# Optimization experiments

Measured on AMD Instinct MI355X. Metric: run time of the kernel, lower is better.

The kernel has to match this reference:

```python
import jax, jax.numpy as jnp
import numpy as np

N_NODES = 50000
N_EDGES = 800000
NUM_RELATIONS = 8   # 2 * n_speakers**2 with n_speakers = 2
NUM_BASES = 30
G_DIM, H1_DIM, H2_DIM = 128, 128, 128


def setup_inputs() -> dict:
    key = jax.random.key(0)
    ks = jax.random.split(key, 10)
    inp = {
        "node_features": jax.random.normal(ks[0], (N_NODES, G_DIM), jnp.float32),
        "edge_index": jax.random.randint(ks[1], (2, N_EDGES), 0, N_NODES, dtype=jnp.int64),
        "edge_type": jax.random.randint(ks[2], (N_EDGES,), 0, NUM_RELATIONS, dtype=jnp.int64),
        "edge_norm": jax.random.uniform(ks[3], (N_EDGES,), jnp.float32),
        # RGCNConv params (basis decomposition)
        "basis": jax.random.normal(ks[4], (NUM_BASES, G_DIM, H1_DIM), jnp.float32) * 0.05,
        "comp": jax.random.normal(ks[5], (NUM_RELATIONS, NUM_BASES), jnp.float32) * 0.1,
        "root": jax.random.normal(ks[6], (G_DIM, H1_DIM), jnp.float32) * 0.05,
        "bias1": jnp.zeros((H1_DIM,), jnp.float32),
        # GraphConv params: lin_rel (with bias) applied to aggregated neighbors, lin_root (no bias)
        "w_rel": jax.random.normal(ks[7], (H1_DIM, H2_DIM), jnp.float32) * 0.05,
        "b_rel": jnp.zeros((H2_DIM,), jnp.float32),
        "w_root": jax.random.normal(ks[8], (H1_DIM, H2_DIM), jnp.float32) * 0.05,
    }
    return inp


def reference(node_features, edge_index, edge_type, edge_norm,
              basis, comp, root, bias1, w_rel, b_rel, w_root):
    src, dst = edge_index[0], edge_index[1]  # source_to_target flow (PyG default)

    # ---- Layer 1: RGCNConv with basis decomposition ----
    # W[r] = sum_b comp[r,b] * basis[b]  -> [R, g, h1]
    W = jnp.einsum('rb,bio->rio', comp, basis)
    # Project every node under every relation once (N*R*h1), then gather per edge.
    # Mathematically identical to per-edge x_j @ W[edge_type] but avoids an [E, g, h1] tensor.
    x_proj = jnp.einsum('ni,rio->nro', node_features, W)  # [N, R, h1]
    msg = x_proj[src, edge_type] * edge_norm[:, None]     # [E, h1]
    agg = jax.ops.segment_sum(msg, dst, num_segments=N_NODES)  # scatter-add to targets
    h = agg + node_features @ root + bias1                # [N, h1]

    # ---- Layer 2: GraphConv (aggr='add', no edge_weight) ----
    agg2 = jax.ops.segment_sum(h[src], dst, num_segments=N_NODES)  # [N, h1]
    out = agg2 @ w_rel + b_rel + h @ w_root               # [N, h2]
    return out
```

## Files before the change

### kernel.cpp

```cpp
#include <hip/hip_runtime.h>
#include <hip/hip_bf16.h>
#include <stdint.h>

#define N_NODES 50000
#define N_EDGES 800000
#define NREL    8
#define NBASES  30
#define DIM     128
#define NSLOT   9
#define NCAT    (NSLOT*DIM)
#define SCAN_NB ((N_NODES + 255) / 256)
#define NB_C    196
#define EPB_PLACE 2048
#define NBLK_PLACE ((N_EDGES + EPB_PLACE - 1) / EPB_PLACE)

typedef __attribute__((ext_vector_type(8))) short short8;
typedef __attribute__((ext_vector_type(4))) float floatx4;
typedef __hip_bfloat16  bf16;
typedef __hip_bfloat162 bf16x2;

__device__ inline ushort f2bu(float f) { bf16 b = __float2bfloat16(f); return *(ushort*)&b; }
__device__ inline float  bu2f(ushort u) { union { unsigned i; float f; } c; c.i = ((unsigned)u) << 16; return c.f; }

__global__ void prep_weights(const float* __restrict__ basis, const float* __restrict__ comp,
                             const float* __restrict__ root, const float* __restrict__ w_rel,
                             const float* __restrict__ w_root,
                             bf16* __restrict__ WcatT, bf16* __restrict__ wrelT, bf16* __restrict__ wrootT) {
    int idx = blockIdx.x * blockDim.x + threadIdx.x;
    const int n_cat = NCAT * DIM;
    const int n_sq  = DIM * DIM;
    if (idx < n_cat) {
        int k = idx & 127, n = idx >> 7;
        int r = n >> 7, o = n & 127;
        float v;
        if (r < NREL) {
            v = 0.f;
            for (int b = 0; b < NBASES; ++b)
                v += comp[r * NBASES + b] * basis[(b * DIM + k) * DIM + o];
        } else {
            v = root[k * DIM + o];
        }
        WcatT[n * DIM + k] = __float2bfloat16(v);
    } else if (idx < n_cat + n_sq) {
        int t = idx - n_cat; int k = t & 127, o = t >> 7;
        wrelT[o * DIM + k] = __float2bfloat16(w_rel[k * DIM + o]);
    } else if (idx < n_cat + 2 * n_sq) {
        int t = idx - n_cat - n_sq; int k = t & 127, o = t >> 7;
        wrootT[o * DIM + k] = __float2bfloat16(w_root[k * DIM + o]);
    }
}

__global__ void conv_x(const float4* __restrict__ x4, ushort4* __restrict__ xb4, int n4) {
    int i = blockIdx.x * blockDim.x + threadIdx.x;
    if (i < n4) {
        float4 f = x4[i];
        ushort4 o;
        o.x = f2bu(f.x); o.y = f2bu(f.y); o.z = f2bu(f.z); o.w = f2bu(f.w);
        xb4[i] = o;
    }
}

__global__ void hist_kernel(const int* __restrict__ ei, int* __restrict__ deg) {
    int e = blockIdx.x * blockDim.x + threadIdx.x;
    if (e < N_EDGES) atomicAdd(&deg[ei[N_EDGES + e]], 1);
}

__global__ void scan_blocks(const int* __restrict__ deg, int* __restrict__ segoff,
                            int* __restrict__ bsum, int n) {
    __shared__ int buf[256];
    int tid = threadIdx.x;
    int i = blockIdx.x * 256 + tid;
    int v = (i < n) ? deg[i] : 0;
    buf[tid] = v;
    __syncthreads();
#pragma unroll
    for (int o = 1; o < 256; o <<= 1) {
        int t = (tid >= o) ? buf[tid - o] : 0;
        __syncthreads();
        buf[tid] += t;
        __syncthreads();
    }
    if (i < n) segoff[i + 1] = buf[tid];
    if (tid == 255) bsum[blockIdx.x] = buf[255];
}

__global__ void scan_sums(int* __restrict__ bsum, int nb) {
    int lane = threadIdx.x;
    int base = 0;
    for (int start = 0; start < nb; start += 64) {
        int i = start + lane;
        int v = (i < nb) ? bsum[i] : 0;
        int incl = v;
#pragma unroll
        for (int o = 1; o < 64; o <<= 1) {
            int t = __shfl_up(incl, o, 64);
            if (lane >= o) incl += t;
        }
        if (i < nb) bsum[i] = base + incl - v;
        base += __shfl(incl, 63, 64);
    }
}

__global__ void scan_add(int* __restrict__ segoff, const int* __restrict__ bsum, int n) {
    int i = blockIdx.x * 256 + threadIdx.x;
    if (i < n) segoff[i + 1] += bsum[blockIdx.x];
    if (i == 0) segoff[0] = 0;
}

__global__ __launch_bounds__(256) void place_kernel(const int* __restrict__ ei, const int* __restrict__ et,
                                                    const float* __restrict__ en, const int* __restrict__ segoff,
                                                    int* __restrict__ bcur, uint2* __restrict__ tmp) {
    __shared__ int lhist[NB_C];
    __shared__ int lbase[NB_C];
    __shared__ int lrank[NB_C];
    int tid = threadIdx.x;
    for (int i = tid; i < NB_C; i += 256) { lhist[i] = 0; lrank[i] = 0; }
    __syncthreads();
    int e0 = blockIdx.x * EPB_PLACE;
#pragma unroll
    for (int i = 0; i < EPB_PLACE / 256; ++i) {
        int e = e0 + i * 256 + tid;
        if (e < N_EDGES) atomicAdd(&lhist[ei[N_EDGES + e] >> 8], 1);
    }
    __syncthreads();
    for (int c = tid; c < NB_C; c += 256)
        if (lhist[c] > 0) lbase[c] = atomicAdd(&bcur[c], lhist[c]);
    __syncthreads();
#pragma unroll
    for (int i = 0; i < EPB_PLACE / 256; ++i) {
        int e = e0 + i * 256 + tid;
        if (e < N_EDGES) {
            int d = ei[N_EDGES + e];
            int c = d >> 8;
            int r = atomicAdd(&lrank[c], 1);
            int p = segoff[c << 8] + lbase[c] + r;
            tmp[p] = make_uint2((unsigned)ei[e] | ((unsigned)et[e] << 16) | ((unsigned)(d & 255) << 19),
                                __float_as_uint(en[e]));
        }
    }
}

__global__ __launch_bounds__(256) void sortb_kernel(const uint2* __restrict__ tmp, const int* __restrict__ segoff,
                                                    uint2* __restrict__ rec) {
    __shared__ int cur[256];
    int c = blockIdx.x;
    int tid = threadIdx.x;
    cur[tid] = 0;
    __syncthreads();
    int base = segoff[c << 8];
    int nlimit = (c + 1) << 8; if (nlimit > N_NODES) nlimit = N_NODES;
    int end = segoff[nlimit];
    for (int i = base + tid; i < end; i += 256) {
        uint2 r = tmp[i];
        int dl = (r.x >> 19) & 255;
        int p = segoff[(c << 8) + dl] + atomicAdd(&cur[dl], 1);
        rec[p] = make_uint2(r.x & 0x7FFFFu, r.y);
    }
}

__global__ __launch_bounds__(256) void gemm1_kernel(const bf16* __restrict__ A, const bf16* __restrict__ BT,
                                                    bf16* __restrict__ C, int M) {
    __shared__ ushort As[64][136];
    __shared__ ushort Bs[64][136];
    const ushort* Au = (const ushort*)A;
    const ushort* Bu = (const ushort*)BT;
    ushort* Cu = (ushort*)C;
    int tm = blockIdx.x * 64;
    int wave = threadIdx.x >> 6, lane = threadIdx.x & 63;
    int q = lane >> 4, mr = lane & 15;

#pragma unroll
    for (int u = 0; u < 4; ++u) {
        int cc = threadIdx.x + u * 256;
        int row = cc >> 4, seg = cc & 15;
        int gr = tm + row;
        short8 av = {0, 0, 0, 0, 0, 0, 0, 0};
        if (gr < M) av = *(const short8*)(Au + (size_t)gr * 128 + seg * 8);
        *(short8*)(&As[row][seg * 8]) = av;
    }

    floatx4 zero = {0.f, 0.f, 0.f, 0.f};
    for (int t = 0; t < 18; ++t) {
        if (t) __syncthreads();
#pragma unroll
        for (int u = 0; u < 4; ++u) {
            int cc = threadIdx.x + u * 256;
            int row = cc >> 4, seg = cc & 15;
            short8 bv = *(const short8*)(Bu + (size_t)(t * 64 + row) * 128 + seg * 8);
            *(short8*)(&Bs[row][seg * 8]) = bv;
        }
        __syncthreads();
        floatx4 acc[4] = {zero, zero, zero, zero};
#pragma unroll
        for (int kt = 0; kt < 4; ++kt) {
            short8 a = *(const short8*)(&As[wave * 16 + mr][q * 8 + kt * 32]);
#pragma unroll
            for (int nt = 0; nt < 4; ++nt) {
                short8 b = *(const short8*)(&Bs[nt * 16 + mr][q * 8 + kt * 32]);
                acc[nt] = __builtin_amdgcn_mfma_f32_16x16x32_bf16(a, b, acc[nt], 0, 0, 0);
            }
        }
#pragma unroll
        for (int nt = 0; nt < 4; ++nt)
#pragma unroll
            for (int r4 = 0; r4 < 4; ++r4) {
                int row = tm + wave * 16 + q * 4 + r4;
                if (row < M) Cu[(size_t)row * NCAT + t * 64 + nt * 16 + mr] = f2bu(acc[nt][r4]);
            }
    }
}

__global__ void seg1_kernel(const uint2* __restrict__ rec, const int* __restrict__ segoff,
                            const ushort* __restrict__ proj, const float* __restrict__ bias1,
                            ushort* __restrict__ h) {
    int quad = threadIdx.x >> 4;
    int node = blockIdx.x * 16 + quad;
    if (node >= N_NODES) return;
    int lane = threadIdx.x & 15;
    int s = segoff[node], e = segoff[node + 1];
    float acc[8] = {0.f, 0.f, 0.f, 0.f, 0.f, 0.f, 0.f, 0.f};
    for (int chunk = s; chunk < e; chunk += 4) {
        int m = e - chunk; if (m > 4) m = 4;
        uint2 rr[4]; short8 vv[4];
#pragma unroll
        for (int j = 0; j < 4; ++j) if (j < m) rr[j] = rec[chunk + j];
#pragma unroll
        for (int j = 0; j < 4; ++j) if (j < m) {
            unsigned src = rr[j].x & 0xFFFFu;
            unsigned typ = rr[j].x >> 16;
            vv[j] = *(const short8*)(proj + ((size_t)src * NSLOT + typ) * 128 + lane * 8);
        }
#pragma unroll
        for (int j = 0; j < 4; ++j) if (j < m) {
            float norm = __uint_as_float(rr[j].y);
#pragma unroll
            for (int f = 0; f < 8; ++f) acc[f] += norm * bu2f((ushort)vv[j][f]);
        }
    }
    short8 base = *(const short8*)(proj + ((size_t)node * NSLOT + 8) * 128 + lane * 8);
    short8 o;
#pragma unroll
    for (int f = 0; f < 8; ++f)
        o[f] = (short)f2bu(acc[f] + bu2f((ushort)base[f]) + bias1[lane * 8 + f]);
    *(short8*)(h + (size_t)node * 128 + lane * 8) = o;
}

__global__ void seg2_kernel(const uint2* __restrict__ rec, const int* __restrict__ segoff,
                            const ushort* __restrict__ h, ushort* __restrict__ out2) {
    int quad = threadIdx.x >> 4;
    int node = blockIdx.x * 16 + quad;
    if (node >= N_NODES) return;
    int lane = threadIdx.x & 15;
    int s = segoff[node], e = segoff[node + 1];
    float acc[8] = {0.f, 0.f, 0.f, 0.f, 0.f, 0.f, 0.f, 0.f};
    for (int chunk = s; chunk < e; chunk += 4) {
        int m = e - chunk; if (m > 4) m = 4;
        uint2 rr[4]; short8 vv[4];
#pragma unroll
        for (int j = 0; j < 4; ++j) if (j < m) rr[j] = rec[chunk + j];
#pragma unroll
        for (int j = 0; j < 4; ++j) if (j < m)
            vv[j] = *(const short8*)(h + (size_t)(rr[j].x & 0xFFFFu) * 128 + lane * 8);
#pragma unroll
        for (int j = 0; j < 4; ++j) if (j < m)
#pragma unroll
            for (int f = 0; f < 8; ++f) acc[f] += bu2f((ushort)vv[j][f]);
    }
    short8 o;
#pragma unroll
    for (int f = 0; f < 8; ++f) o[f] = (short)f2bu(acc[f]);
    *(short8*)(out2 + (size_t)node * 128 + lane * 8) = o;
}

__global__ __launch_bounds__(256) void gemm2_kernel(const bf16* __restrict__ A1, const bf16* __restrict__ B1T,
                                                    const bf16* __restrict__ A2, const bf16* __restrict__ B2T,
                                                    const float* __restrict__ brel, float* __restrict__ out, int M) {
    __shared__ ushort As[64][136];
    __shared__ ushort Bs[64][136];
    int tm = blockIdx.x * 64, tn = blockIdx.y * 64;
    int wave = threadIdx.x >> 6, lane = threadIdx.x & 63;
    int q = lane >> 4, mr = lane & 15;
    floatx4 zero = {0.f, 0.f, 0.f, 0.f};
    floatx4 acc[4] = {zero, zero, zero, zero};

    for (int phase = 0; phase < 2; ++phase) {
        const ushort* Au = (const ushort*)(phase ? A2 : A1);
        const ushort* Bu = (const ushort*)(phase ? B2T : B1T);
        if (phase) __syncthreads();
        for (int c = threadIdx.x; c < 64 * 16; c += 256) {
            int row = c >> 4, seg = c & 15;
            int gr = tm + row;
            short8 av = {0, 0, 0, 0, 0, 0, 0, 0};
            if (gr < M) av = *(const short8*)(Au + (size_t)gr * 128 + seg * 8);
            *(short8*)(&As[row][seg * 8]) = av;
            short8 bv = *(const short8*)(Bu + (size_t)(tn + row) * 128 + seg * 8);
            *(short8*)(&Bs[row][seg * 8]) = bv;
        }
        __syncthreads();
#pragma unroll
        for (int kt = 0; kt < 4; ++kt) {
            short8 a = *(const short8*)(&As[wave * 16 + mr][q * 8 + kt * 32]);
#pragma unroll
            for (int nt = 0; nt < 4; ++nt) {
                short8 b = *(const short8*)(&Bs[nt * 16 + mr][q * 8 + kt * 32]);
                acc[nt] = __builtin_amdgcn_mfma_f32_16x16x32_bf16(a, b, acc[nt], 0, 0, 0);
            }
        }
    }
    __syncthreads();
    float* Csf = (float*)&As[0][0];
#pragma unroll
    for (int nt = 0; nt < 4; ++nt)
#pragma unroll
        for (int r4 = 0; r4 < 4; ++r4) {
            int row = wave * 16 + q * 4 + r4;
            int col = nt * 16 + mr;
            Csf[row * 68 + col] = acc[nt][r4] + brel[tn + col];
        }
    __syncthreads();
#pragma unroll
    for (int u = 0; u < 4; ++u) {
        int cc = threadIdx.x + u * 256;
        int row = cc >> 4, seg = cc & 15;
        int gr = tm + row;
        if (gr < M) {
            float4 v = *(const float4*)(&Csf[row * 68 + seg * 4]);
            *(float4*)(out + (size_t)gr * 128 + tn + seg * 4) = v;
        }
    }
}

extern "C" void kernel_launch(void* const* d_in, const int* in_sizes, int n_in,
                              void* d_out, int out_size, void* d_ws, size_t ws_size,
                              hipStream_t stream) {
    const float* x      = (const float*)d_in[0];
    const int*   ei     = (const int*)d_in[1];
    const int*   et     = (const int*)d_in[2];
    const float* en     = (const float*)d_in[3];
    const float* basis  = (const float*)d_in[4];
    const float* comp   = (const float*)d_in[5];
    const float* root   = (const float*)d_in[6];
    const float* bias1  = (const float*)d_in[7];
    const float* w_rel  = (const float*)d_in[8];
    const float* b_rel  = (const float*)d_in[9];
    const float* w_root = (const float*)d_in[10];
    float* out = (float*)d_out;

    char* ws = (char*)d_ws;
    size_t off = 0;
    auto alloc = [&](size_t bytes) { size_t o = off; off += (bytes + 255) & ~(size_t)255; return o; };

    size_t o_deg    = alloc((size_t)N_NODES * 4);
    size_t o_bcur   = alloc((size_t)NB_C * 4);
    size_t o_segoff = alloc((size_t)(N_NODES + 1) * 4);
    size_t o_bsum   = alloc((size_t)SCAN_NB * 4);
    size_t o_rec    = alloc((size_t)N_EDGES * 8);
    size_t o_tmp    = alloc((size_t)N_EDGES * 8);
    size_t o_wcat   = alloc((size_t)NCAT * DIM * 2);
    size_t o_wrel   = alloc((size_t)DIM * DIM * 2);
    size_t o_wroot  = alloc((size_t)DIM * DIM * 2);
    size_t o_xb     = alloc((size_t)N_NODES * DIM * 2);
    size_t o_proj   = alloc((size_t)N_NODES * NCAT * 2);
    size_t o_hb     = alloc((size_t)N_NODES * DIM * 2);
    size_t o_agg2   = alloc((size_t)N_NODES * DIM * 2);

    int*   deg    = (int*)(ws + o_deg);
    int*   bcur   = (int*)(ws + o_bcur);
    int*   segoff = (int*)(ws + o_segoff);
    int*   bsum   = (int*)(ws + o_bsum);
    uint2* rec    = (uint2*)(ws + o_rec);
    uint2* tmp    = (uint2*)(ws + o_tmp);
    bf16*  wcat   = (bf16*)(ws + o_wcat);
    bf16*  wrelT  = (bf16*)(ws + o_wrel);
    bf16*  wrootT = (bf16*)(ws + o_wroot);
    bf16*  xb     = (bf16*)(ws + o_xb);
    bf16*  proj   = (bf16*)(ws + o_proj);
    bf16*  hb     = (bf16*)(ws + o_hb);
    bf16*  agg2   = (bf16*)(ws + o_agg2);

    hipMemsetAsync(ws + o_deg, 0, o_segoff - o_deg, stream);

    {
        int total = NCAT * DIM + 2 * DIM * DIM;
        prep_weights<<<(total + 255) / 256, 256, 0, stream>>>(basis, comp, root, w_rel, w_root,
                                                              wcat, wrelT, wrootT);
    }
    {
        int n4 = N_NODES * DIM / 4;
        conv_x<<<(n4 + 255) / 256, 256, 0, stream>>>((const float4*)x, (ushort4*)xb, n4);
    }
    hist_kernel<<<(N_EDGES + 255) / 256, 256, 0, stream>>>(ei, deg);
    scan_blocks<<<SCAN_NB, 256, 0, stream>>>(deg, segoff, bsum, N_NODES);
    scan_sums<<<1, 64, 0, stream>>>(bsum, SCAN_NB);
    scan_add<<<SCAN_NB, 256, 0, stream>>>(segoff, bsum, N_NODES);
    place_kernel<<<NBLK_PLACE, 256, 0, stream>>>(ei, et, en, segoff, bcur, tmp);
    sortb_kernel<<<NB_C, 256, 0, stream>>>(tmp, segoff, rec);

    gemm1_kernel<<<(N_NODES + 63) / 64, 256, 0, stream>>>(xb, wcat, proj, N_NODES);
    seg1_kernel<<<(N_NODES + 15) / 16, 256, 0, stream>>>(rec, segoff, (const ushort*)proj, bias1, (ushort*)hb);
    seg2_kernel<<<(N_NODES + 15) / 16, 256, 0, stream>>>(rec, segoff, (const ushort*)hb, (ushort*)agg2);
    {
        dim3 grid((N_NODES + 63) / 64, DIM / 64);
        gemm2_kernel<<<grid, 256, 0, stream>>>(agg2, wrelT, hb, wrootT, b_rel, out, N_NODES);
    }
}
```

Measured before the change: 328.6 us.

## Merge setup kernels, use single-pass decoupled scan, co-schedule gemm1 with edge placement

Fuses weight prep, x conversion and degree histogram into one launch. The three-kernel scan becomes a single-pass scan in which each block publishes its total through a flag word and then sums the totals of earlier blocks. The gemm1 tiles and the edge-placement blocks run in one grid so the two independent jobs overlap. This cuts launch count and idle gaps between kernels. The scan's spin-wait depends on earlier blocks being scheduled first, and the fused gemm grid mixes very different block types.

```diff
diff --git a/kernel.cpp b/kernel.cpp
--- a/kernel.cpp
+++ b/kernel.cpp
@@ -13,6 +13,11 @@
 #define NB_C    196
 #define EPB_PLACE 2048
 #define NBLK_PLACE ((N_EDGES + EPB_PLACE - 1) / EPB_PLACE)
+#define GEMM1_TILES ((N_NODES + 63) / 64)
+#define PREP_TOTAL  (NCAT * DIM + 2 * DIM * DIM)
+#define PREP_BLKS   ((PREP_TOTAL + 255) / 256)
+#define CONV_BLKS   ((N_NODES * DIM / 4 + 255) / 256)
+#define HIST_BLKS   ((N_EDGES + 255) / 256)
 
 typedef __attribute__((ext_vector_type(8))) short short8;
 typedef __attribute__((ext_vector_type(4))) float floatx4;
@@ -22,54 +27,57 @@
 __device__ inline ushort f2bu(float f) { bf16 b = __float2bfloat16(f); return *(ushort*)&b; }
 __device__ inline float  bu2f(ushort u) { union { unsigned i; float f; } c; c.i = ((unsigned)u) << 16; return c.f; }
 
-__global__ void prep_weights(const float* __restrict__ basis, const float* __restrict__ comp,
-                             const float* __restrict__ root, const float* __restrict__ w_rel,
-                             const float* __restrict__ w_root,
-                             bf16* __restrict__ WcatT, bf16* __restrict__ wrelT, bf16* __restrict__ wrootT) {
-    int idx = blockIdx.x * blockDim.x + threadIdx.x;
-    const int n_cat = NCAT * DIM;
-    const int n_sq  = DIM * DIM;
-    if (idx < n_cat) {
-        int k = idx & 127, n = idx >> 7;
-        int r = n >> 7, o = n & 127;
-        float v;
-        if (r < NREL) {
-            v = 0.f;
-            for (int b = 0; b < NBASES; ++b)
-                v += comp[r * NBASES + b] * basis[(b * DIM + k) * DIM + o];
-        } else {
-            v = root[k * DIM + o];
-        }
-        WcatT[n * DIM + k] = __float2bfloat16(v);
-    } else if (idx < n_cat + n_sq) {
-        int t = idx - n_cat; int k = t & 127, o = t >> 7;
-        wrelT[o * DIM + k] = __float2bfloat16(w_rel[k * DIM + o]);
-    } else if (idx < n_cat + 2 * n_sq) {
-        int t = idx - n_cat - n_sq; int k = t & 127, o = t >> 7;
-        wrootT[o * DIM + k] = __float2bfloat16(w_root[k * DIM + o]);
-    }
-}
-
-__global__ void conv_x(const float4* __restrict__ x4, ushort4* __restrict__ xb4, int n4) {
-    int i = blockIdx.x * blockDim.x + threadIdx.x;
-    if (i < n4) {
-        float4 f = x4[i];
-        ushort4 o;
-        o.x = f2bu(f.x); o.y = f2bu(f.y); o.z = f2bu(f.z); o.w = f2bu(f.w);
-        xb4[i] = o;
-    }
-}
-
-__global__ void hist_kernel(const int* __restrict__ ei, int* __restrict__ deg) {
-    int e = blockIdx.x * blockDim.x + threadIdx.x;
-    if (e < N_EDGES) atomicAdd(&deg[ei[N_EDGES + e]], 1);
-}
-
-__global__ void scan_blocks(const int* __restrict__ deg, int* __restrict__ segoff,
-                            int* __restrict__ bsum, int n) {
+__global__ __launch_bounds__(256) void setup_kernel(const float* __restrict__ basis, const float* __restrict__ comp,
+                                                    const float* __restrict__ root, const float* __restrict__ w_rel,
+                                                    const float* __restrict__ w_root,
+                                                    bf16* __restrict__ WcatT, bf16* __restrict__ wrelT,
+                                                    bf16* __restrict__ wrootT,
+                                                    const float4* __restrict__ x4, ushort4* __restrict__ xb4,
+                                                    const int* __restrict__ ei, int* __restrict__ deg) {
+    int b = blockIdx.x;
+    if (b < PREP_BLKS) {
+        int idx = b * 256 + threadIdx.x;
+        const int n_cat = NCAT * DIM;
+        const int n_sq  = DIM * DIM;
+        if (idx < n_cat) {
+            int k = idx & 127, n = idx >> 7;
+            int r = n >> 7, o = n & 127;
+            float v;
+            if (r < NREL) {
+                v = 0.f;
+                for (int bb = 0; bb < NBASES; ++bb)
+                    v += comp[r * NBASES + bb] * basis[(bb * DIM + k) * DIM + o];
+            } else {
+                v = root[k * DIM + o];
+            }
+            WcatT[n * DIM + k] = __float2bfloat16(v);
+        } else if (idx < n_cat + n_sq) {
+            int t = idx - n_cat; int k = t & 127, o = t >> 7;
+            wrelT[o * DIM + k] = __float2bfloat16(w_rel[k * DIM + o]);
+        } else if (idx < n_cat + 2 * n_sq) {
+            int t = idx - n_cat - n_sq; int k = t & 127, o = t >> 7;
+            wrootT[o * DIM + k] = __float2bfloat16(w_root[k * DIM + o]);
+        }
+    } else if (b < PREP_BLKS + CONV_BLKS) {
+        int i = (b - PREP_BLKS) * 256 + threadIdx.x;
+        int n4 = N_NODES * DIM / 4;
+        if (i < n4) {
+            float4 f = x4[i];
+            ushort4 o;
+            o.x = f2bu(f.x); o.y = f2bu(f.y); o.z = f2bu(f.z); o.w = f2bu(f.w);
+            xb4[i] = o;
+        }
+    } else {
+        int e = (b - PREP_BLKS - CONV_BLKS) * 256 + threadIdx.x;
+        if (e < N_EDGES) atomicAdd(&deg[ei[N_EDGES + e]], 1);
+    }
+}
+
+__global__ __launch_bounds__(256) void scan_one(const int* __restrict__ deg, int* __restrict__ segoff,
+                                                unsigned long long* __restrict__ bstate, int n) {
     __shared__ int buf[256];
-    int tid = threadIdx.x;
-    int i = blockIdx.x * 256 + tid;
+    int b = blockIdx.x, tid = threadIdx.x;
+    int i = b * 256 + tid;
     int v = (i < n) ? deg[i] : 0;
     buf[tid] = v;
     __syncthreads();
@@ -80,62 +88,116 @@
         buf[tid] += t;
         __syncthreads();
     }
-    if (i < n) segoff[i + 1] = buf[tid];
-    if (tid == 255) bsum[blockIdx.x] = buf[255];
-}
-
-__global__ void scan_sums(int* __restrict__ bsum, int nb) {
-    int lane = threadIdx.x;
-    int base = 0;
-    for (int start = 0; start < nb; start += 64) {
-        int i = start + lane;
-        int v = (i < nb) ? bsum[i] : 0;
-        int incl = v;
-#pragma unroll
-        for (int o = 1; o < 64; o <<= 1) {
-            int t = __shfl_up(incl, o, 64);
-            if (lane >= o) incl += t;
-        }
-        if (i < nb) bsum[i] = base + incl - v;
-        base += __shfl(incl, 63, 64);
-    }
-}
-
-__global__ void scan_add(int* __restrict__ segoff, const int* __restrict__ bsum, int n) {
-    int i = blockIdx.x * 256 + threadIdx.x;
-    if (i < n) segoff[i + 1] += bsum[blockIdx.x];
-    if (i == 0) segoff[0] = 0;
-}
-
-__global__ __launch_bounds__(256) void place_kernel(const int* __restrict__ ei, const int* __restrict__ et,
-                                                    const float* __restrict__ en, const int* __restrict__ segoff,
-                                                    int* __restrict__ bcur, uint2* __restrict__ tmp) {
-    __shared__ int lhist[NB_C];
-    __shared__ int lbase[NB_C];
-    __shared__ int lrank[NB_C];
-    int tid = threadIdx.x;
-    for (int i = tid; i < NB_C; i += 256) { lhist[i] = 0; lrank[i] = 0; }
-    __syncthreads();
-    int e0 = blockIdx.x * EPB_PLACE;
-#pragma unroll
-    for (int i = 0; i < EPB_PLACE / 256; ++i) {
-        int e = e0 + i * 256 + tid;
-        if (e < N_EDGES) atomicAdd(&lhist[ei[N_EDGES + e] >> 8], 1);
-    }
-    __syncthreads();
-    for (int c = tid; c < NB_C; c += 256)
-        if (lhist[c] > 0) lbase[c] = atomicAdd(&bcur[c], lhist[c]);
-    __syncthreads();
-#pragma unroll
-    for (int i = 0; i < EPB_PLACE / 256; ++i) {
-        int e = e0 + i * 256 + tid;
-        if (e < N_EDGES) {
-            int d = ei[N_EDGES + e];
-            int c = d >> 8;
-            int r = atomicAdd(&lrank[c], 1);
-            int p = segoff[c << 8] + lbase[c] + r;
-            tmp[p] = make_uint2((unsigned)ei[e] | ((unsigned)et[e] << 16) | ((unsigned)(d & 255) << 19),
-                                __float_as_uint(en[e]));
+    int incl = buf[tid];
+    int total = buf[255];
+    if (tid == 0)
+        __hip_atomic_store(&bstate[b], (1ULL << 32) | (unsigned)total,
+                           __ATOMIC_RELEASE, __HIP_MEMORY_SCOPE_AGENT);
+    int mysum = 0;
+    for (int j = tid; j < b; j += 256) {
+        unsigned long long s;
+        do {
+            s = __hip_atomic_load(&bstate[j], __ATOMIC_ACQUIRE, __HIP_MEMORY_SCOPE_AGENT);
+        } while (!(s >> 32));
+        mysum += (int)(s & 0xFFFFFFFFu);
+    }
+    __syncthreads();
+    buf[tid] = mysum;
+    __syncthreads();
+#pragma unroll
+    for (int o = 128; o > 0; o >>= 1) {
+        if (tid < o) buf[tid] += buf[tid + o];
+        __syncthreads();
+    }
+    int base = buf[0];
+    if (i < n) segoff[i + 1] = base + incl;
+    if (b == 0 && tid == 0) segoff[0] = 0;
+}
+
+__global__ __launch_bounds__(256) void gemm1_place(const bf16* __restrict__ A, const bf16* __restrict__ BT,
+                                                   bf16* __restrict__ C, int M,
+                                                   const int* __restrict__ ei, const int* __restrict__ et,
+                                                   const float* __restrict__ en, const int* __restrict__ segoff,
+                                                   int* __restrict__ bcur, uint2* __restrict__ tmp) {
+    __shared__ ushort smem[2 * 64 * 136];
+    int blk = blockIdx.x;
+    if (blk < GEMM1_TILES) {
+        ushort (*As)[136] = (ushort(*)[136])smem;
+        ushort (*Bs)[136] = (ushort(*)[136])(smem + 64 * 136);
+        const ushort* Au = (const ushort*)A;
+        const ushort* Bu = (const ushort*)BT;
+        ushort* Cu = (ushort*)C;
+        int tm = blk * 64;
+        int wave = threadIdx.x >> 6, lane = threadIdx.x & 63;
+        int q = lane >> 4, mr = lane & 15;
+
+#pragma unroll
+        for (int u = 0; u < 4; ++u) {
+            int cc = threadIdx.x + u * 256;
+            int row = cc >> 4, seg = cc & 15;
+            int gr = tm + row;
+            short8 av = {0, 0, 0, 0, 0, 0, 0, 0};
+            if (gr < M) av = *(const short8*)(Au + (size_t)gr * 128 + seg * 8);
+            *(short8*)(&As[row][seg * 8]) = av;
+        }
+
+        floatx4 zero = {0.f, 0.f, 0.f, 0.f};
+        for (int t = 0; t < 18; ++t) {
+            if (t) __syncthreads();
+#pragma unroll
+            for (int u = 0; u < 4; ++u) {
+                int cc = threadIdx.x + u * 256;
+                int row = cc >> 4, seg = cc & 15;
+                short8 bv = *(const short8*)(Bu + (size_t)(t * 64 + row) * 128 + seg * 8);
+                *(short8*)(&Bs[row][seg * 8]) = bv;
+            }
+            __syncthreads();
+            floatx4 acc[4] = {zero, zero, zero, zero};
+#pragma unroll
+            for (int kt = 0; kt < 4; ++kt) {
+                short8 a = *(const short8*)(&As[wave * 16 + mr][q * 8 + kt * 32]);
+#pragma unroll
+                for (int nt = 0; nt < 4; ++nt) {
+                    short8 bb = *(const short8*)(&Bs[nt * 16 + mr][q * 8 + kt * 32]);
+                    acc[nt] = __builtin_amdgcn_mfma_f32_16x16x32_bf16(a, bb, acc[nt], 0, 0, 0);
+                }
+            }
+#pragma unroll
+            for (int nt = 0; nt < 4; ++nt)
+#pragma unroll
+                for (int r4 = 0; r4 < 4; ++r4) {
+                    int row = tm + wave * 16 + q * 4 + r4;
+                    if (row < M) Cu[(size_t)row * NCAT + t * 64 + nt * 16 + mr] = f2bu(acc[nt][r4]);
+                }
+        }
+    } else {
+        int* lhist = (int*)smem;
+        int* lbase = lhist + NB_C;
+        int* lrank = lbase + NB_C;
+        int tid = threadIdx.x;
+        for (int i = tid; i < NB_C; i += 256) { lhist[i] = 0; lrank[i] = 0; }
+        __syncthreads();
+        int e0 = (blk - GEMM1_TILES) * EPB_PLACE;
+#pragma unroll
+        for (int i = 0; i < EPB_PLACE / 256; ++i) {
+            int e = e0 + i * 256 + tid;
+            if (e < N_EDGES) atomicAdd(&lhist[ei[N_EDGES + e] >> 8], 1);
+        }
+        __syncthreads();
+        for (int c = tid; c < NB_C; c += 256)
+            if (lhist[c] > 0) lbase[c] = atomicAdd(&bcur[c], lhist[c]);
+        __syncthreads();
+#pragma unroll
+        for (int i = 0; i < EPB_PLACE / 256; ++i) {
+            int e = e0 + i * 256 + tid;
+            if (e < N_EDGES) {
+                int d = ei[N_EDGES + e];
+                int c = d >> 8;
+                int r = atomicAdd(&lrank[c], 1);
+                int p = segoff[c << 8] + lbase[c] + r;
+                tmp[p] = make_uint2((unsigned)ei[e] | ((unsigned)et[e] << 16) | ((unsigned)(d & 255) << 19),
+                                    __float_as_uint(en[e]));
+            }
         }
     }
 }
@@ -155,58 +217,6 @@
         int dl = (r.x >> 19) & 255;
         int p = segoff[(c << 8) + dl] + atomicAdd(&cur[dl], 1);
         rec[p] = make_uint2(r.x & 0x7FFFFu, r.y);
-    }
-}
-
-__global__ __launch_bounds__(256) void gemm1_kernel(const bf16* __restrict__ A, const bf16* __restrict__ BT,
-                                                    bf16* __restrict__ C, int M) {
-    __shared__ ushort As[64][136];
-    __shared__ ushort Bs[64][136];
-    const ushort* Au = (const ushort*)A;
-    const ushort* Bu = (const ushort*)BT;
-    ushort* Cu = (ushort*)C;
-    int tm = blockIdx.x * 64;
-    int wave = threadIdx.x >> 6, lane = threadIdx.x & 63;
-    int q = lane >> 4, mr = lane & 15;
-
-#pragma unroll
-    for (int u = 0; u < 4; ++u) {
-        int cc = threadIdx.x + u * 256;
-        int row = cc >> 4, seg = cc & 15;
-        int gr = tm + row;
-        short8 av = {0, 0, 0, 0, 0, 0, 0, 0};
-        if (gr < M) av = *(const short8*)(Au + (size_t)gr * 128 + seg * 8);
-        *(short8*)(&As[row][seg * 8]) = av;
-    }
-
-    floatx4 zero = {0.f, 0.f, 0.f, 0.f};
-    for (int t = 0; t < 18; ++t) {
-        if (t) __syncthreads();
-#pragma unroll
-        for (int u = 0; u < 4; ++u) {
-            int cc = threadIdx.x + u * 256;
-            int row = cc >> 4, seg = cc & 15;
-            short8 bv = *(const short8*)(Bu + (size_t)(t * 64 + row) * 128 + seg * 8);
-            *(short8*)(&Bs[row][seg * 8]) = bv;
-        }
-        __syncthreads();
-        floatx4 acc[4] = {zero, zero, zero, zero};
-#pragma unroll
-        for (int kt = 0; kt < 4; ++kt) {
-            short8 a = *(const short8*)(&As[wave * 16 + mr][q * 8 + kt * 32]);
-#pragma unroll
-            for (int nt = 0; nt < 4; ++nt) {
-                short8 b = *(const short8*)(&Bs[nt * 16 + mr][q * 8 + kt * 32]);
-                acc[nt] = __builtin_amdgcn_mfma_f32_16x16x32_bf16(a, b, acc[nt], 0, 0, 0);
-            }
-        }
-#pragma unroll
-        for (int nt = 0; nt < 4; ++nt)
-#pragma unroll
-            for (int r4 = 0; r4 < 4; ++r4) {
-                int row = tm + wave * 16 + q * 4 + r4;
-                if (row < M) Cu[(size_t)row * NCAT + t * 64 + nt * 16 + mr] = f2bu(acc[nt][r4]);
-            }
     }
 }
 
@@ -352,8 +362,8 @@
 
     size_t o_deg    = alloc((size_t)N_NODES * 4);
     size_t o_bcur   = alloc((size_t)NB_C * 4);
+    size_t o_bstate = alloc((size_t)SCAN_NB * 8);
     size_t o_segoff = alloc((size_t)(N_NODES + 1) * 4);
-    size_t o_bsum   = alloc((size_t)SCAN_NB * 4);
     size_t o_rec    = alloc((size_t)N_EDGES * 8);
     size_t o_tmp    = alloc((size_t)N_EDGES * 8);
     size_t o_wcat   = alloc((size_t)NCAT * DIM * 2);
@@ -366,8 +376,8 @@
 
     int*   deg    = (int*)(ws + o_deg);
     int*   bcur   = (int*)(ws + o_bcur);
+    unsigned long long* bstate = (unsigned long long*)(ws + o_bstate);
     int*   segoff = (int*)(ws + o_segoff);
-    int*   bsum   = (int*)(ws + o_bsum);
     uint2* rec    = (uint2*)(ws + o_rec);
     uint2* tmp    = (uint2*)(ws + o_tmp);
     bf16*  wcat   = (bf16*)(ws + o_wcat);
@@ -380,23 +390,13 @@
 
     hipMemsetAsync(ws + o_deg, 0, o_segoff - o_deg, stream);
 
-    {
-        int total = NCAT * DIM + 2 * DIM * DIM;
-        prep_weights<<<(total + 255) / 256, 256, 0, stream>>>(basis, comp, root, w_rel, w_root,
-                                                              wcat, wrelT, wrootT);
-    }
-    {
-        int n4 = N_NODES * DIM / 4;
-        conv_x<<<(n4 + 255) / 256, 256, 0, stream>>>((const float4*)x, (ushort4*)xb, n4);
-    }
-    hist_kernel<<<(N_EDGES + 255) / 256, 256, 0, stream>>>(ei, deg);
-    scan_blocks<<<SCAN_NB, 256, 0, stream>>>(deg, segoff, bsum, N_NODES);
-    scan_sums<<<1, 64, 0, stream>>>(bsum, SCAN_NB);
-    scan_add<<<SCAN_NB, 256, 0, stream>>>(segoff, bsum, N_NODES);
-    place_kernel<<<NBLK_PLACE, 256, 0, stream>>>(ei, et, en, segoff, bcur, tmp);
+    setup_kernel<<<PREP_BLKS + CONV_BLKS + HIST_BLKS, 256, 0, stream>>>(
+        basis, comp, root, w_rel, w_root, wcat, wrelT, wrootT,
+        (const float4*)x, (ushort4*)xb, ei, deg);
+    scan_one<<<SCAN_NB, 256, 0, stream>>>(deg, segoff, bstate, N_NODES);
+    gemm1_place<<<GEMM1_TILES + NBLK_PLACE, 256, 0, stream>>>(xb, wcat, proj, N_NODES,
+                                                              ei, et, en, segoff, bcur, tmp);
     sortb_kernel<<<NB_C, 256, 0, stream>>>(tmp, segoff, rec);
-
-    gemm1_kernel<<<(N_NODES + 63) / 64, 256, 0, stream>>>(xb, wcat, proj, N_NODES);
     seg1_kernel<<<(N_NODES + 15) / 16, 256, 0, stream>>>(rec, segoff, (const ushort*)proj, bias1, (ushort*)hb);
     seg2_kernel<<<(N_NODES + 15) / 16, 256, 0, stream>>>(rec, segoff, (const ushort*)hb, (ushort*)agg2);
     {
```

Result: no change. 326.8 us (-0.6%).
